# Optimization experiments

Hardware: AMD Instinct MI355X
Metric: run time of the kernel (lower is better)

Reference implementation:

```python
import jax, jax.numpy as jnp
import numpy as np

DIM = 768
H = 12
DH = DIM // H          # 64
ROPE_DIM = (DH // 6) * 6   # 60
HALF = (ROPE_DIM // 3) // 2  # 10 freqs per axis
THETA = 10000.0
EPS = 1e-6


def rmsnorm(x, w):
    xf = x.astype(jnp.float32)
    var = jnp.mean(xf * xf, axis=-1, keepdims=True)
    return (w * (xf * jax.lax.rsqrt(var + EPS))).astype(x.dtype)


def rope_angles(positions):
    # positions: [B, N, 3] -> angles [B, N, 3*HALF]
    freqs = 1.0 / (THETA ** (jnp.arange(HALF, dtype=jnp.float32) / HALF))  # [HALF]
    # [B,N,3,1] * [1,1,1,HALF] -> [B,N,3,HALF] -> concat over axis order x,y,z
    ang = positions[..., :, None] * freqs[None, None, None, :]
    return ang.reshape(*positions.shape[:2], 3 * HALF)  # [B,N,30]


def apply_rope(t, cos, sin):
    # t: [B,N,H,ROPE_DIM]; cos/sin: [B,N,1,ROPE_DIM//2]
    B, N, Hh, D = t.shape
    tf = t.astype(jnp.float32).reshape(B, N, Hh, D // 2, 2)
    te, to = tf[..., 0], tf[..., 1]
    oe = te * cos - to * sin
    oo = te * sin + to * cos
    return jnp.stack([oe, oo], axis=-1).reshape(B, N, Hh, D).astype(t.dtype)


def setup_inputs() -> dict:
    key = jax.random.key(0)
    ks = jax.random.split(key, 5)
    B, N = 2, 2048
    x = jax.random.normal(ks[0], (B, N, DIM), dtype=jnp.float32)
    positions = jax.random.uniform(ks[1], (B, N, 3), dtype=jnp.float32)
    qkv_w = jax.random.normal(ks[2], (3 * DIM, DIM), dtype=jnp.float32) * (DIM ** -0.5)
    proj_w = jax.random.normal(ks[3], (DIM, DIM), dtype=jnp.float32) * (DIM ** -0.5)
    proj_b = jnp.zeros((DIM,), dtype=jnp.float32)
    qn_w = jnp.ones((DH,), dtype=jnp.float32)
    kn_w = jnp.ones((DH,), dtype=jnp.float32)
    return {"x": x, "positions": positions, "qkv_w": qkv_w, "proj_w": proj_w,
            "proj_b": proj_b, "qn_w": qn_w, "kn_w": kn_w}


def reference(x, positions, qkv_w, proj_w, proj_b, qn_w, kn_w):
    B, N, C = x.shape
    scale = DH ** -0.5
    qkv = (x @ qkv_w.T).reshape(B, N, 3, H, DH)
    q, k, v = qkv[:, :, 0], qkv[:, :, 1], qkv[:, :, 2]  # [B,N,H,DH]
    q = rmsnorm(q, qn_w)
    k = rmsnorm(k, kn_w)
    # 3D RoPE on first ROPE_DIM channels
    ang = rope_angles(positions)                 # [B,N,30]
    cos = jnp.cos(ang)[:, :, None, :]            # [B,N,1,30]
    sin = jnp.sin(ang)[:, :, None, :]
    q = jnp.concatenate([apply_rope(q[..., :ROPE_DIM], cos, sin), q[..., ROPE_DIM:]], axis=-1)
    k = jnp.concatenate([apply_rope(k[..., :ROPE_DIM], cos, sin), k[..., ROPE_DIM:]], axis=-1)
    attn = jnp.einsum('bqhd,bkhd->bhqk', q, k) * scale  # [B,H,N,N]
    attn = jax.nn.softmax(attn, axis=-1)
    out = jnp.einsum('bhqk,bkhd->bqhd', attn, v).reshape(B, N, C)
    return out @ proj_w.T + proj_b
```

## Files before the change

### kernel.cpp

```cpp
#include <hip/hip_runtime.h>
#include <hip/hip_bf16.h>
#include <math.h>

#define DIM 768
#define NH 12
#define DH 64
#define SEQ 2048
#define BATCH 2
#define TOK (BATCH*SEQ)
#define QKVN (3*DIM)

typedef __attribute__((ext_vector_type(8))) short bf16x8;
typedef __attribute__((ext_vector_type(4))) float f32x4;
typedef __attribute__((ext_vector_type(2))) unsigned int u32x2;
typedef unsigned short u16;

#define VM0 asm volatile("s_waitcnt vmcnt(0)" ::: "memory")
#define VM2 asm volatile("s_waitcnt vmcnt(2)" ::: "memory")
#define VM4 asm volatile("s_waitcnt vmcnt(4)" ::: "memory")
#define LGKM0 asm volatile("s_waitcnt lgkmcnt(0)" ::: "memory")
#define BAR() __builtin_amdgcn_s_barrier()

__device__ inline u16 f2bf(float f) {
  union { float f; unsigned u; } v; v.f = f;
  unsigned u = v.u;
  u += 0x7fffu + ((u >> 16) & 1u);
  return (u16)(u >> 16);
}

__device__ inline int pkbf(float a, float b) {
  __hip_bfloat162 h = __float22bfloat162_rn(make_float2(a, b));
  int r; __builtin_memcpy(&r, &h, 4); return r;
}

__global__ void conv_all(const float* __restrict__ a, u16* __restrict__ ao, int na4,
                         const float* __restrict__ b, u16* __restrict__ bo, int nb4,
                         const float* __restrict__ c, u16* __restrict__ co, int nc4,
                         const float* __restrict__ pos, float2* __restrict__ tab) {
  int i4 = blockIdx.x * blockDim.x + threadIdx.x;
  const int nconv = na4 + nb4 + nc4;
  if (i4 < nconv) {
    const float* src; u16* dst; int off;
    if (i4 < na4)            { src = a; dst = ao; off = i4; }
    else if (i4 < na4 + nb4) { src = b; dst = bo; off = i4 - na4; }
    else                     { src = c; dst = co; off = i4 - na4 - nb4; }
    float4 v = ((const float4*)src)[off];
    ushort4 o;
    o.x = f2bf(v.x); o.y = f2bf(v.y); o.z = f2bf(v.z); o.w = f2bf(v.w);
    ((ushort4*)dst)[off] = o;
    return;
  }
  int e = i4 - nconv;
  if (e >= TOK * 32) return;
  int t = e >> 5, p = e & 31;
  float cs = 1.f, sn = 0.f;
  if (p < 30) {
    int axis = p / 10, fi = p % 10;
    float freq = exp2f(-(float)fi * 1.3287712379549449f);
    float ang = pos[t * 3 + axis] * freq;
    cs = cosf(ang); sn = sinf(ang);
  }
  tab[e] = make_float2(cs, sn);
}

#define GLL(g, s) __builtin_amdgcn_global_load_lds((const __attribute__((address_space(1))) void*)(g), (__attribute__((address_space(3))) void*)(s), 16, 0, 0)

__global__ __launch_bounds__(256, 6) void gemm64(
    const u16* __restrict__ A, const u16* __restrict__ W,
    float* __restrict__ C, const float* __restrict__ bias,
    int M, int Nn, int K)
{
  __shared__ u16 As[2][64 * 32];
  __shared__ u16 Bs[2][64 * 32];
  const int t = threadIdx.x;
  const int w = t >> 6, l = t & 63;
  const int lr = l & 15, lg = l >> 4;
  const int wr = w >> 1, wc = w & 1;
  const int m0 = blockIdx.x * 64;
  const int n0 = blockIdx.y * 64;
  f32x4 acc[2][2] = {};
  const int srow = t >> 2;
  const int scol = (t & 3) * 8;
  const u16* aSrc = A + (size_t)(m0 + srow) * K + scol;
  const u16* bSrc = W + (size_t)(n0 + srow) * K + scol;
  const int NT = K / 32;

  GLL(aSrc, &As[0][w * 512]);
  GLL(bSrc, &Bs[0][w * 512]);

  for (int kt = 0; kt < NT; ++kt) {
    const int cur = kt & 1;
    if (kt + 1 < NT) {
      GLL(aSrc + (kt + 1) * 32, &As[cur ^ 1][w * 512]);
      GLL(bSrc + (kt + 1) * 32, &Bs[cur ^ 1][w * 512]);
      VM2;
    } else {
      VM0;
    }
    BAR();
    bf16x8 af[2], bff[2];
#pragma unroll
    for (int mi = 0; mi < 2; ++mi)
      af[mi] = *(const bf16x8*)(&As[cur][0] + (wr * 32 + mi * 16 + lr) * 32 + lg * 8);
#pragma unroll
    for (int ni = 0; ni < 2; ++ni)
      bff[ni] = *(const bf16x8*)(&Bs[cur][0] + (wc * 32 + ni * 16 + lr) * 32 + lg * 8);
#pragma unroll
    for (int mi = 0; mi < 2; ++mi)
#pragma unroll
      for (int ni = 0; ni < 2; ++ni)
        acc[mi][ni] = __builtin_amdgcn_mfma_f32_16x16x32_bf16(af[mi], bff[ni], acc[mi][ni], 0, 0, 0);
    LGKM0;
    BAR();
  }

#pragma unroll
  for (int mi = 0; mi < 2; ++mi)
#pragma unroll
    for (int ni = 0; ni < 2; ++ni)
#pragma unroll
      for (int r = 0; r < 4; ++r) {
        int row = m0 + wr * 32 + mi * 16 + lg * 4 + r;
        int col = n0 + wc * 32 + ni * 16 + lr;
        C[(size_t)row * Nn + col] = acc[mi][ni][r] + bias[col];
      }
}

__global__ __launch_bounds__(512, 4) void gemm_qkv(
    const u16* __restrict__ A, const u16* __restrict__ W,
    const float* __restrict__ qn_w, const float* __restrict__ kn_w,
    const float2* __restrict__ tab,
    u16* __restrict__ Qb, u16* __restrict__ Kb, u16* __restrict__ Vtb)
{
  __shared__ u16 As[2][128 * 32];
  __shared__ u16 Bs[2][128 * 32];
  const int K = DIM;
  const int t = threadIdx.x;
  const int w = t >> 6, l = t & 63;
  const int lr = l & 15, lg = l >> 4;
  const int wr = w >> 1, wc = w & 1;
  const int m0 = blockIdx.x * 128;
  const int n0 = blockIdx.y * 128;
  f32x4 acc[2][4] = {};
  const int srow = t >> 2;
  const int scol = (t & 3) * 8;
  const u16* aSrc = A + (size_t)(m0 + srow) * K + scol;
  const u16* bSrc = W + (size_t)(n0 + srow) * K + scol;
  const int NT = K / 32;

  GLL(aSrc, &As[0][w * 512]);
  GLL(bSrc, &Bs[0][w * 512]);

  for (int kt = 0; kt < NT; ++kt) {
    const int cur = kt & 1;
    if (kt + 1 < NT) {
      GLL(aSrc + (kt + 1) * 32, &As[cur ^ 1][w * 512]);
      GLL(bSrc + (kt + 1) * 32, &Bs[cur ^ 1][w * 512]);
      VM2;
    } else {
      VM0;
    }
    BAR();
    bf16x8 af[2], bff[4];
#pragma unroll
    for (int mi = 0; mi < 2; ++mi)
      af[mi] = *(const bf16x8*)(&As[cur][0] + (wr * 32 + mi * 16 + lr) * 32 + lg * 8);
#pragma unroll
    for (int ni = 0; ni < 4; ++ni)
      bff[ni] = *(const bf16x8*)(&Bs[cur][0] + (wc * 64 + ni * 16 + lr) * 32 + lg * 8);
#pragma unroll
    for (int mi = 0; mi < 2; ++mi)
#pragma unroll
      for (int ni = 0; ni < 4; ++ni)
        acc[mi][ni] = __builtin_amdgcn_mfma_f32_16x16x32_bf16(af[mi], bff[ni], acc[mi][ni], 0, 0, 0);
    LGKM0;
    BAR();
  }

  const int chunk = (n0 >> 6) + wc;
  const int tt = chunk / 12;
  const int h  = chunk % 12;
  const int bB = m0 >> 11;
  const int bh = bB * NH + h;

  if (tt == 2) {
#pragma unroll
    for (int mi = 0; mi < 2; ++mi) {
      const int nbase = (m0 + wr * 32 + mi * 16 + lg * 4) & 2047;
#pragma unroll
      for (int ni = 0; ni < 4; ++ni) {
        const int d = ni * 16 + lr;
        ushort4 o;
        o.x = f2bf(acc[mi][ni][0]); o.y = f2bf(acc[mi][ni][1]);
        o.z = f2bf(acc[mi][ni][2]); o.w = f2bf(acc[mi][ni][3]);
        *(ushort4*)(Vtb + ((size_t)bh * DH + d) * SEQ + nbase) = o;
      }
    }
  } else {
    const float* wv = (tt == 0 ? qn_w : kn_w);
    const float qs = (tt == 0 ? 0.125f * 1.4426950408889634f : 1.f);
    float wgt[4];
#pragma unroll
    for (int ni = 0; ni < 4; ++ni) wgt[ni] = wv[ni * 16 + lr];
    u16* outp = (tt == 0 ? Qb : Kb) + (size_t)bh * SEQ * DH;
#pragma unroll
    for (int mi = 0; mi < 2; ++mi) {
#pragma unroll
      for (int r = 0; r < 4; ++r) {
        float ss = 0.f;
#pragma unroll
        for (int ni = 0; ni < 4; ++ni) ss += acc[mi][ni][r] * acc[mi][ni][r];
        ss += __shfl_xor(ss, 1, 64);
        ss += __shfl_xor(ss, 2, 64);
        ss += __shfl_xor(ss, 4, 64);
        ss += __shfl_xor(ss, 8, 64);
        const float rms = rsqrtf(ss * (1.f / 64.f) + 1e-6f);
        const int trow = m0 + wr * 32 + mi * 16 + lg * 4 + r;
        const float2* tl = tab + trow * 32;
        u16* rowp = outp + (size_t)(trow & 2047) * DH;
#pragma unroll
        for (int ni = 0; ni < 4; ++ni) {
          const int d = ni * 16 + lr;
          float v = acc[mi][ni][r] * rms * wgt[ni];
          float vp = __shfl_xor(v, 1, 64);
          float2 cssn = tl[ni * 8 + (lr >> 1)];
          float sgn = (d & 1) ? cssn.y : -cssn.y;
          rowp[d] = f2bf((v * cssn.x + vp * sgn) * qs);
        }
      }
    }
  }
}

__global__ __launch_bounds__(512, 6) void attn(
    const u16* __restrict__ Qb, const u16* __restrict__ Kb,
    const u16* __restrict__ Vtb, u16* __restrict__ Ob)
{
  __shared__ u16 Ks[2][2][64 * 64];
  __shared__ u16 Vs[2][64 * 64];
  const int tid = threadIdx.x;
  const int w = tid >> 6, l = tid & 63;
  const int lr = l & 15, lg = l >> 4;
  const int qg = w & 3, half = w >> 2;
  const int wg = blockIdx.x;
  const int swz = (wg & 7) * 96 + (wg >> 3);
  const int bh = swz >> 5;
  const int q0 = (swz & 31) * 64;
  const u16* Qp = Qb + (size_t)bh * SEQ * DH;
  const u16* Kp = Kb + (size_t)bh * SEQ * DH;
  const u16* Vp = Vtb + (size_t)bh * DH * SEQ;

  const int qrow = q0 + qg * 16 + lr;
  const bf16x8 bq0 = *(const bf16x8*)(Qp + (size_t)qrow * DH + 8 * lg);
  const bf16x8 bq1 = *(const bf16x8*)(Qp + (size_t)qrow * DH + 32 + 8 * lg);

  const int srow = tid >> 3;
  const int sc16 = (tid & 7) ^ (srow & 7);
  const u16* kSrc = Kp + (size_t)srow * DH + sc16 * 8;
  const u16* vSrc = Vp + (size_t)srow * SEQ + sc16 * 8;

  const int frow = (lr & 3) | ((lr & 4) << 1) | ((lr & 8) >> 1);
  const int ksw = frow & 7;
  const int vsw = lr & 7;

  f32x4 oacc[4] = {};
  float lsum = 0.f;

  GLL(kSrc,        &Ks[0][0][w * 512]);
  GLL(kSrc + 4096, &Ks[0][1][w * 512]);
  GLL(vSrc,        &Vs[0][w * 512]);
  GLL(vSrc + 64,   &Vs[1][w * 512]);

  for (int i = 0; i < 16; ++i) {
    const int p = i & 1;
    if (i + 1 < 16) {
      const size_t ko = (size_t)(2 * i + 2) * 4096;
      GLL(kSrc + ko,        &Ks[p ^ 1][0][w * 512]);
      GLL(kSrc + ko + 4096, &Ks[p ^ 1][1][w * 512]);
      VM4;
    } else {
      VM2;
    }
    BAR();
    const u16* Kt = &Ks[p][half][0];
    const u16* Vt = &Vs[half][0];

    f32x4 pacc[4] = {};
    __builtin_amdgcn_s_setprio(1);
#pragma unroll
    for (int c = 0; c < 4; ++c) {
      const int rbase = (16 * c + frow) * 64;
      bf16x8 ka = *(const bf16x8*)(Kt + rbase + ((lg ^ ksw) * 8));
      bf16x8 kb = *(const bf16x8*)(Kt + rbase + (((4 + lg) ^ ksw) * 8));
      pacc[c] = __builtin_amdgcn_mfma_f32_16x16x32_bf16(ka, bq0, pacc[c], 0, 0, 0);
      pacc[c] = __builtin_amdgcn_mfma_f32_16x16x32_bf16(kb, bq1, pacc[c], 0, 0, 0);
    }
    __builtin_amdgcn_s_setprio(0);
    float pp[4][4];
#pragma unroll
    for (int c = 0; c < 4; ++c)
#pragma unroll
      for (int r = 0; r < 4; ++r) {
        float pv = __builtin_amdgcn_exp2f(pacc[c][r] - 12.f);
        pp[c][r] = pv;
        lsum += pv;
      }

    if (i + 1 < 16) { VM2; } else { VM0; }
    LGKM0;
    BAR();

#pragma unroll
    for (int g = 0; g < 2; ++g) {
      const int clo = 2 * g, chi = 2 * g + 1;
      unsigned x01 = (unsigned)pkbf(pp[clo][0], pp[clo][1]);
      unsigned x23 = (unsigned)pkbf(pp[clo][2], pp[clo][3]);
      unsigned y01 = (unsigned)pkbf(pp[chi][0], pp[chi][1]);
      unsigned y23 = (unsigned)pkbf(pp[chi][2], pp[chi][3]);
      u32x2 r0 = __builtin_amdgcn_permlane32_swap(x01, y01, false, false);
      u32x2 r1 = __builtin_amdgcn_permlane32_swap(x23, y23, false, false);
      union { unsigned d[4]; bf16x8 v; } pu;
      pu.d[0] = r0[0]; pu.d[1] = r1[0]; pu.d[2] = r0[1]; pu.d[3] = r1[1];
      __builtin_amdgcn_s_setprio(1);
#pragma unroll
      for (int dt = 0; dt < 4; ++dt) {
        bf16x8 va = *(const bf16x8*)(Vt + (16 * dt + lr) * 64 + (((4 * g + lg) ^ vsw) * 8));
        oacc[dt] = __builtin_amdgcn_mfma_f32_16x16x32_bf16(va, pu.v, oacc[dt], 0, 0, 0);
      }
      __builtin_amdgcn_s_setprio(0);
    }

    LGKM0;
    BAR();

    if (i + 1 < 16) {
      const size_t vo = (size_t)(2 * i + 2) * 64;
      GLL(vSrc + vo,      &Vs[0][w * 512]);
      GLL(vSrc + vo + 64, &Vs[1][w * 512]);
    }
  }

  float* scr = (float*)&Ks[0][0][0];
  const int sid = qg * 64 + l;
  if (half == 1) {
#pragma unroll
    for (int dt = 0; dt < 4; ++dt)
#pragma unroll
      for (int r = 0; r < 4; ++r)
        scr[sid * 17 + dt * 4 + r] = oacc[dt][r];
    scr[sid * 17 + 16] = lsum;
  }
  __syncthreads();
  if (half == 1) return;
#pragma unroll
  for (int dt = 0; dt < 4; ++dt)
#pragma unroll
    for (int r = 0; r < 4; ++r)
      oacc[dt][r] += scr[sid * 17 + dt * 4 + r];
  lsum += scr[sid * 17 + 16];

  lsum += __shfl_xor(lsum, 16, 64);
  lsum += __shfl_xor(lsum, 32, 64);
  const float inv = 1.f / lsum;
  const int b = bh / NH, h = bh % NH;
  const int q = q0 + qg * 16 + lr;
  size_t obase = (size_t)(b * SEQ + q) * DIM + h * DH + 4 * lg;
#pragma unroll
  for (int dt = 0; dt < 4; ++dt) {
    ushort4 o;
    o.x = f2bf(oacc[dt][0] * inv);
    o.y = f2bf(oacc[dt][1] * inv);
    o.z = f2bf(oacc[dt][2] * inv);
    o.w = f2bf(oacc[dt][3] * inv);
    *(ushort4*)(Ob + obase + 16 * dt) = o;
  }
}

extern "C" void kernel_launch(void* const* d_in, const int* in_sizes, int n_in,
                              void* d_out, int out_size, void* d_ws, size_t ws_size,
                              hipStream_t stream) {
  const float* x      = (const float*)d_in[0];
  const float* pos    = (const float*)d_in[1];
  const float* qkv_w  = (const float*)d_in[2];
  const float* proj_w = (const float*)d_in[3];
  const float* proj_b = (const float*)d_in[4];
  const float* qn_w   = (const float*)d_in[5];
  const float* kn_w   = (const float*)d_in[6];
  char* ws = (char*)d_ws;
  u16*    xb    = (u16*)(ws + 0);
  u16*    wqkv  = (u16*)(ws + 6291456);
  u16*    wproj = (u16*)(ws + 9830400);
  float2* tab   = (float2*)(ws + 11010048);
  u16*    Qb    = (u16*)(ws + 12058624);
  u16*    Kb    = (u16*)(ws + 18350080);
  u16*    Vtb   = (u16*)(ws + 24641536);
  u16*    Ob    = (u16*)(ws + 30932992);
  float* out = (float*)d_out;

  const int na4 = TOK * DIM / 4, nb4 = QKVN * DIM / 4, nc4 = DIM * DIM / 4;
  const int ntot = na4 + nb4 + nc4 + TOK * 32;
  conv_all<<<(ntot + 255) / 256, 256, 0, stream>>>(
      x, xb, na4, qkv_w, wqkv, nb4, proj_w, wproj, nc4, pos, tab);

  dim3 g1(TOK / 128, QKVN / 128);
  gemm_qkv<<<g1, 512, 0, stream>>>(xb, wqkv, qn_w, kn_w, tab, Qb, Kb, Vtb);

  attn<<<SEQ / 64 * BATCH * NH, 512, 0, stream>>>(Qb, Kb, Vtb, Ob);

  dim3 g3(TOK / 64, DIM / 64);
  gemm64<<<g3, 256, 0, stream>>>(Ob, wproj, out, proj_b, TOK, DIM, DIM);
}
```

Before: 94.25 us.

## Halve attention block to 256 threads with two query tiles per wave

The attention kernel now runs 4 waves per block instead of 8. Each wave handles two 16-row query tiles, so every K and V fragment read from LDS feeds twice as many MFMAs. To keep the same 64-row staging, each thread issues twice as many global-to-LDS loads, and the wait counts are adjusted to match. The softmax row sum now comes from an MFMA against a vector of ones instead of scalar adds plus cross-lane shuffles. This raises register pressure and halves the number of waves per block, which may reduce latency hiding.

```diff
diff --git a/kernel.cpp b/kernel.cpp
--- a/kernel.cpp
+++ b/kernel.cpp
@@ -18,6 +18,7 @@
 #define VM0 asm volatile("s_waitcnt vmcnt(0)" ::: "memory")
 #define VM2 asm volatile("s_waitcnt vmcnt(2)" ::: "memory")
 #define VM4 asm volatile("s_waitcnt vmcnt(4)" ::: "memory")
+#define VM8 asm volatile("s_waitcnt vmcnt(8)" ::: "memory")
 #define LGKM0 asm volatile("s_waitcnt lgkmcnt(0)" ::: "memory")
 #define BAR() __builtin_amdgcn_s_barrier()
 
@@ -232,7 +233,7 @@
   }
 }
 
-__global__ __launch_bounds__(512, 6) void attn(
+__global__ __launch_bounds__(256, 3) void attn(
     const u16* __restrict__ Qb, const u16* __restrict__ Kb,
     const u16* __restrict__ Vtb, u16* __restrict__ Ob)
 {
@@ -241,7 +242,7 @@
   const int tid = threadIdx.x;
   const int w = tid >> 6, l = tid & 63;
   const int lr = l & 15, lg = l >> 4;
-  const int qg = w & 3, half = w >> 2;
+  const int qg = w & 1, half = w >> 1;
   const int wg = blockIdx.x;
   const int swz = (wg & 7) * 96 + (wg >> 3);
   const int bh = swz >> 5;
@@ -250,9 +251,11 @@
   const u16* Kp = Kb + (size_t)bh * SEQ * DH;
   const u16* Vp = Vtb + (size_t)bh * DH * SEQ;
 
-  const int qrow = q0 + qg * 16 + lr;
-  const bf16x8 bq0 = *(const bf16x8*)(Qp + (size_t)qrow * DH + 8 * lg);
-  const bf16x8 bq1 = *(const bf16x8*)(Qp + (size_t)qrow * DH + 32 + 8 * lg);
+  const int qrA = q0 + qg * 32 + lr;
+  const bf16x8 bq0a = *(const bf16x8*)(Qp + (size_t)qrA * DH + 8 * lg);
+  const bf16x8 bq1a = *(const bf16x8*)(Qp + (size_t)qrA * DH + 32 + 8 * lg);
+  const bf16x8 bq0b = *(const bf16x8*)(Qp + (size_t)(qrA + 16) * DH + 8 * lg);
+  const bf16x8 bq1b = *(const bf16x8*)(Qp + (size_t)(qrA + 16) * DH + 32 + 8 * lg);
 
   const int srow = tid >> 3;
   const int sc16 = (tid & 7) ^ (srow & 7);
@@ -263,70 +266,87 @@
   const int ksw = frow & 7;
   const int vsw = lr & 7;
 
-  f32x4 oacc[4] = {};
-  float lsum = 0.f;
-
-  GLL(kSrc,        &Ks[0][0][w * 512]);
-  GLL(kSrc + 4096, &Ks[0][1][w * 512]);
-  GLL(vSrc,        &Vs[0][w * 512]);
-  GLL(vSrc + 64,   &Vs[1][w * 512]);
+  bf16x8 vone;
+#pragma unroll
+  for (int j = 0; j < 8; ++j) vone[j] = (short)0x3F80;
+
+  f32x4 oaccA[4] = {}, oaccB[4] = {};
+  f32x4 laccA = {}, laccB = {};
+
+  GLL(kSrc,          &Ks[0][0][w * 512]);
+  GLL(kSrc + 2048,   &Ks[0][0][w * 512 + 2048]);
+  GLL(kSrc + 4096,   &Ks[0][1][w * 512]);
+  GLL(kSrc + 6144,   &Ks[0][1][w * 512 + 2048]);
+  GLL(vSrc,          &Vs[0][w * 512]);
+  GLL(vSrc + 65536,  &Vs[0][w * 512 + 2048]);
+  GLL(vSrc + 64,     &Vs[1][w * 512]);
+  GLL(vSrc + 64 + 65536, &Vs[1][w * 512 + 2048]);
 
   for (int i = 0; i < 16; ++i) {
     const int p = i & 1;
     if (i + 1 < 16) {
       const size_t ko = (size_t)(2 * i + 2) * 4096;
       GLL(kSrc + ko,        &Ks[p ^ 1][0][w * 512]);
+      GLL(kSrc + ko + 2048, &Ks[p ^ 1][0][w * 512 + 2048]);
       GLL(kSrc + ko + 4096, &Ks[p ^ 1][1][w * 512]);
+      GLL(kSrc + ko + 6144, &Ks[p ^ 1][1][w * 512 + 2048]);
+      VM8;
+    } else {
       VM4;
-    } else {
-      VM2;
     }
     BAR();
     const u16* Kt = &Ks[p][half][0];
     const u16* Vt = &Vs[half][0];
 
-    f32x4 pacc[4] = {};
+    f32x4 paccA[4] = {}, paccB[4] = {};
     __builtin_amdgcn_s_setprio(1);
 #pragma unroll
     for (int c = 0; c < 4; ++c) {
       const int rbase = (16 * c + frow) * 64;
       bf16x8 ka = *(const bf16x8*)(Kt + rbase + ((lg ^ ksw) * 8));
       bf16x8 kb = *(const bf16x8*)(Kt + rbase + (((4 + lg) ^ ksw) * 8));
-      pacc[c] = __builtin_amdgcn_mfma_f32_16x16x32_bf16(ka, bq0, pacc[c], 0, 0, 0);
-      pacc[c] = __builtin_amdgcn_mfma_f32_16x16x32_bf16(kb, bq1, pacc[c], 0, 0, 0);
+      paccA[c] = __builtin_amdgcn_mfma_f32_16x16x32_bf16(ka, bq0a, paccA[c], 0, 0, 0);
+      paccA[c] = __builtin_amdgcn_mfma_f32_16x16x32_bf16(kb, bq1a, paccA[c], 0, 0, 0);
+      paccB[c] = __builtin_amdgcn_mfma_f32_16x16x32_bf16(ka, bq0b, paccB[c], 0, 0, 0);
+      paccB[c] = __builtin_amdgcn_mfma_f32_16x16x32_bf16(kb, bq1b, paccB[c], 0, 0, 0);
     }
     __builtin_amdgcn_s_setprio(0);
-    float pp[4][4];
-#pragma unroll
-    for (int c = 0; c < 4; ++c)
-#pragma unroll
-      for (int r = 0; r < 4; ++r) {
-        float pv = __builtin_amdgcn_exp2f(pacc[c][r] - 12.f);
-        pp[c][r] = pv;
-        lsum += pv;
-      }
-
-    if (i + 1 < 16) { VM2; } else { VM0; }
+
+    if (i + 1 < 16) { VM4; } else { VM0; }
     LGKM0;
     BAR();
 
 #pragma unroll
     for (int g = 0; g < 2; ++g) {
       const int clo = 2 * g, chi = 2 * g + 1;
-      unsigned x01 = (unsigned)pkbf(pp[clo][0], pp[clo][1]);
-      unsigned x23 = (unsigned)pkbf(pp[clo][2], pp[clo][3]);
-      unsigned y01 = (unsigned)pkbf(pp[chi][0], pp[chi][1]);
-      unsigned y23 = (unsigned)pkbf(pp[chi][2], pp[chi][3]);
-      u32x2 r0 = __builtin_amdgcn_permlane32_swap(x01, y01, false, false);
-      u32x2 r1 = __builtin_amdgcn_permlane32_swap(x23, y23, false, false);
-      union { unsigned d[4]; bf16x8 v; } pu;
-      pu.d[0] = r0[0]; pu.d[1] = r1[0]; pu.d[2] = r0[1]; pu.d[3] = r1[1];
+      float pA[8], pB[8];
+#pragma unroll
+      for (int r = 0; r < 4; ++r) {
+        pA[r]     = __builtin_amdgcn_exp2f(paccA[clo][r] - 12.f);
+        pA[4 + r] = __builtin_amdgcn_exp2f(paccA[chi][r] - 12.f);
+        pB[r]     = __builtin_amdgcn_exp2f(paccB[clo][r] - 12.f);
+        pB[4 + r] = __builtin_amdgcn_exp2f(paccB[chi][r] - 12.f);
+      }
+      u32x2 a0 = __builtin_amdgcn_permlane32_swap((unsigned)pkbf(pA[0], pA[1]),
+                                                  (unsigned)pkbf(pA[4], pA[5]), false, false);
+      u32x2 a1 = __builtin_amdgcn_permlane32_swap((unsigned)pkbf(pA[2], pA[3]),
+                                                  (unsigned)pkbf(pA[6], pA[7]), false, false);
+      u32x2 b0 = __builtin_amdgcn_permlane32_swap((unsigned)pkbf(pB[0], pB[1]),
+                                                  (unsigned)pkbf(pB[4], pB[5]), false, false);
+      u32x2 b1 = __builtin_amdgcn_permlane32_swap((unsigned)pkbf(pB[2], pB[3]),
+                                                  (unsigned)pkbf(pB[6], pB[7]), false, false);
+      union { unsigned d[4]; bf16x8 v; } puA, puB;
+      puA.d[0] = a0[0]; puA.d[1] = a1[0]; puA.d[2] = a0[1]; puA.d[3] = a1[1];
+      puB.d[0] = b0[0]; puB.d[1] = b1[0]; puB.d[2] = b0[1]; puB.d[3] = b1[1];
       __builtin_amdgcn_s_setprio(1);
 #pragma unroll
       for (int dt = 0; dt < 4; ++dt) {
         bf16x8 va = *(const bf16x8*)(Vt + (16 * dt + lr) * 64 + (((4 * g + lg) ^ vsw) * 8));
-        oacc[dt] = __builtin_amdgcn_mfma_f32_16x16x32_bf16(va, pu.v, oacc[dt], 0, 0, 0);
-      }
+        oaccA[dt] = __builtin_amdgcn_mfma_f32_16x16x32_bf16(va, puA.v, oaccA[dt], 0, 0, 0);
+        oaccB[dt] = __builtin_amdgcn_mfma_f32_16x16x32_bf16(va, puB.v, oaccB[dt], 0, 0, 0);
+      }
+      laccA = __builtin_amdgcn_mfma_f32_16x16x32_bf16(vone, puA.v, laccA, 0, 0, 0);
+      laccB = __builtin_amdgcn_mfma_f32_16x16x32_bf16(vone, puB.v, laccB, 0, 0, 0);
       __builtin_amdgcn_s_setprio(0);
     }
 
@@ -335,44 +355,52 @@
 
     if (i + 1 < 16) {
       const size_t vo = (size_t)(2 * i + 2) * 64;
-      GLL(vSrc + vo,      &Vs[0][w * 512]);
-      GLL(vSrc + vo + 64, &Vs[1][w * 512]);
+      GLL(vSrc + vo,              &Vs[0][w * 512]);
+      GLL(vSrc + vo + 65536,      &Vs[0][w * 512 + 2048]);
+      GLL(vSrc + vo + 64,         &Vs[1][w * 512]);
+      GLL(vSrc + vo + 64 + 65536, &Vs[1][w * 512 + 2048]);
     }
   }
 
   float* scr = (float*)&Ks[0][0][0];
-  const int sid = qg * 64 + l;
+  const int sidA = (qg * 2 + 0) * 64 + l;
+  const int sidB = (qg * 2 + 1) * 64 + l;
   if (half == 1) {
 #pragma unroll
     for (int dt = 0; dt < 4; ++dt)
 #pragma unroll
-      for (int r = 0; r < 4; ++r)
-        scr[sid * 17 + dt * 4 + r] = oacc[dt][r];
-    scr[sid * 17 + 16] = lsum;
+      for (int r = 0; r < 4; ++r) {
+        scr[sidA * 17 + dt * 4 + r] = oaccA[dt][r];
+        scr[sidB * 17 + dt * 4 + r] = oaccB[dt][r];
+      }
+    scr[sidA * 17 + 16] = laccA[0];
+    scr[sidB * 17 + 16] = laccB[0];
   }
   __syncthreads();
   if (half == 1) return;
 #pragma unroll
   for (int dt = 0; dt < 4; ++dt)
 #pragma unroll
-    for (int r = 0; r < 4; ++r)
-      oacc[dt][r] += scr[sid * 17 + dt * 4 + r];
-  lsum += scr[sid * 17 + 16];
-
-  lsum += __shfl_xor(lsum, 16, 64);
-  lsum += __shfl_xor(lsum, 32, 64);
-  const float inv = 1.f / lsum;
+    for (int r = 0; r < 4; ++r) {
+      oaccA[dt][r] += scr[sidA * 17 + dt * 4 + r];
+      oaccB[dt][r] += scr[sidB * 17 + dt * 4 + r];
+    }
+  const float invA = 1.f / (laccA[0] + scr[sidA * 17 + 16]);
+  const float invB = 1.f / (laccB[0] + scr[sidB * 17 + 16]);
+
   const int b = bh / NH, h = bh % NH;
-  const int q = q0 + qg * 16 + lr;
-  size_t obase = (size_t)(b * SEQ + q) * DIM + h * DH + 4 * lg;
+  const int qA = q0 + qg * 32 + lr;
+  size_t obA = (size_t)(b * SEQ + qA) * DIM + h * DH + 4 * lg;
+  size_t obB = (size_t)(b * SEQ + qA + 16) * DIM + h * DH + 4 * lg;
 #pragma unroll
   for (int dt = 0; dt < 4; ++dt) {
-    ushort4 o;
-    o.x = f2bf(oacc[dt][0] * inv);
-    o.y = f2bf(oacc[dt][1] * inv);
-    o.z = f2bf(oacc[dt][2] * inv);
-    o.w = f2bf(oacc[dt][3] * inv);
-    *(ushort4*)(Ob + obase + 16 * dt) = o;
+    ushort4 oA, oB;
+    oA.x = f2bf(oaccA[dt][0] * invA); oA.y = f2bf(oaccA[dt][1] * invA);
+    oA.z = f2bf(oaccA[dt][2] * invA); oA.w = f2bf(oaccA[dt][3] * invA);
+    oB.x = f2bf(oaccB[dt][0] * invB); oB.y = f2bf(oaccB[dt][1] * invB);
+    oB.z = f2bf(oaccB[dt][2] * invB); oB.w = f2bf(oaccB[dt][3] * invB);
+    *(ushort4*)(Ob + obA + 16 * dt) = oA;
+    *(ushort4*)(Ob + obB + 16 * dt) = oB;
   }
 }
 
@@ -405,7 +433,7 @@
   dim3 g1(TOK / 128, QKVN / 128);
   gemm_qkv<<<g1, 512, 0, stream>>>(xb, wqkv, qn_w, kn_w, tab, Qb, Kb, Vtb);
 
-  attn<<<SEQ / 64 * BATCH * NH, 512, 0, stream>>>(Qb, Kb, Vtb, Ob);
+  attn<<<SEQ / 64 * BATCH * NH, 256, 0, stream>>>(Qb, Kb, Vtb, Ob);
 
   dim3 g3(TOK / 64, DIM / 64);
   gemm64<<<g3, 256, 0, stream>>>(Ob, wproj, out, proj_b, TOK, DIM, DIM);
```

After: 91.69 us. 2.7% less time.
